# Kernel optimization log

Measured on AMD Instinct MI355X. Metric: run time of the kernel, lower is better.

Reference implementation:

```python
import jax, jax.numpy as jnp
import numpy as np

B, SIZE, TRACK = 4096, 1024, 1024  # batch, input size, tracker_size


def setup_inputs() -> dict:
    key = jax.random.key(0)
    ks = jax.random.split(key, 9)
    s = 0.02  # small init scale to keep gates in a sane range
    return {
        "top_buf_h": jax.random.normal(ks[0], (B, SIZE), jnp.float32),
        "top_stack1_h": jax.random.normal(ks[1], (B, SIZE), jnp.float32),
        "top_stack2_h": jax.random.normal(ks[2], (B, SIZE), jnp.float32),
        "h_prev": jax.random.normal(ks[3], (B, TRACK), jnp.float32),
        "c_prev": jax.random.normal(ks[4], (B, TRACK), jnp.float32),
        "W_buf": jax.random.normal(ks[5], (SIZE, 4 * TRACK), jnp.float32) * s,
        "W_stack1": jax.random.normal(ks[6], (SIZE, 4 * TRACK), jnp.float32) * s,
        "W_stack2": jax.random.normal(ks[7], (SIZE, 4 * TRACK), jnp.float32) * s,
        "W_lateral": jax.random.normal(ks[8], (TRACK, 4 * TRACK), jnp.float32) * s,
        "b_lateral": jnp.zeros((4 * TRACK,), jnp.float32),
    }


def reference(top_buf_h, top_stack1_h, top_stack2_h, h_prev, c_prev,
              W_buf, W_stack1, W_stack2, W_lateral, b_lateral):
    # Fused tracker step: 3 bias-free projections + lateral projection (with bias)
    gates = (top_buf_h @ W_buf
             + top_stack1_h @ W_stack1
             + top_stack2_h @ W_stack2
             + h_prev @ W_lateral
             + b_lateral)                      # [B, 4*TRACK]
    # SPINN lstm(c_prev, gates): chunk order (a, i, f, o)
    a, i, f, o = jnp.split(gates, 4, axis=1)
    c = jnp.tanh(a) * jax.nn.sigmoid(i) + jax.nn.sigmoid(f) * c_prev
    h = jax.nn.sigmoid(o) * jnp.tanh(c)
    return (h, c)
```

## Files before the change

kernel.cpp:

```cpp
#include <hip/hip_runtime.h>


typedef __bf16 bf16x8 __attribute__((ext_vector_type(8)));
typedef float  f32x4  __attribute__((ext_vector_type(4)));

__device__ __forceinline__ unsigned short f2bf(float x) {
    unsigned int u = __builtin_bit_cast(unsigned int, x);
    u = (u + 0x7fffu + ((u >> 16) & 1u)) >> 16;
    return (unsigned short)u;
}

__device__ __forceinline__ void gl2lds16(const unsigned short* g, unsigned short* l) {
    __builtin_amdgcn_global_load_lds(
        (const __attribute__((address_space(1))) unsigned int*)g,
        (__attribute__((address_space(3))) unsigned int*)l,
        16, 0, 0);
}

__device__ __forceinline__ float sigf(float x) {
    return __builtin_amdgcn_rcpf(1.f + __expf(-x));
}
__device__ __forceinline__ float tanh_fast(float x) {
    return 2.f * __builtin_amdgcn_rcpf(1.f + __expf(-2.f * x)) - 1.f;
}


__global__ void convert_AB(const float* __restrict__ A0, const float* __restrict__ A1,
                           const float* __restrict__ A2, const float* __restrict__ A3,
                           const float* __restrict__ Wb, const float* __restrict__ W1,
                           const float* __restrict__ W2, const float* __restrict__ Wl,
                           unsigned short* __restrict__ Abf,
                           unsigned short* __restrict__ Bt) {
    __shared__ float t[32][33];
    if (blockIdx.x < 16384) {
        int idx = blockIdx.x * 256 + threadIdx.x;
        int e0  = idx * 4;
        int b   = e0 >> 12;
        int k   = e0 & 4095;
        const float* S = (k < 1024) ? A0 : (k < 2048) ? A1 : (k < 3072) ? A2 : A3;
        int col = k & 1023;
        const float4 v = *reinterpret_cast<const float4*>(S + (size_t)b * 1024 + col);
        ushort4 o;
        o.x = f2bf(v.x); o.y = f2bf(v.y); o.z = f2bf(v.z); o.w = f2bf(v.w);
        *reinterpret_cast<ushort4*>(Abf + (size_t)b * 4096 + k) = o;
    } else {
        int tile = blockIdx.x - 16384;
        int jt = tile & 127, kt = tile >> 7;
        int j0 = jt * 32, k0 = kt * 32;
        int ksel = k0 >> 10;
        const float* S = (ksel == 0) ? Wb : (ksel == 1) ? W1 : (ksel == 2) ? W2 : Wl;
        int kloc = k0 & 1023;
        int tx = threadIdx.x & 31, ty = threadIdx.x >> 5;
#pragma unroll
        for (int i = 0; i < 4; ++i) {
            int r = ty + i * 8;
            t[r][tx] = S[(size_t)(kloc + r) * 4096 + j0 + tx];
        }
        __syncthreads();
        int g = j0 >> 10;
        int nbase = j0 & 1023;
#pragma unroll
        for (int i = 0; i < 4; ++i) {
            int jj = ty + i * 8;
            int u  = nbase + jj;
            int p  = (u >> 6) * 256 + ((u >> 4) & 3) * 64 + g * 16 + (u & 15);
            Bt[(size_t)p * 4096 + k0 + tx] = f2bf(t[tx][jj]);
        }
    }
}


__global__ __launch_bounds__(512, 2) void gemm_lstm(
        const unsigned short* __restrict__ A,
        const unsigned short* __restrict__ Bt,
        const float* __restrict__ bias,
        const float* __restrict__ cprev,
        float* __restrict__ out) {
    __shared__ unsigned short lds[65536];
#define ASB(b) (lds + (b) * 16384)
#define BSB(b) (lds + 32768 + (b) * 16384)

    const int tid  = threadIdx.x;
    const int wid  = tid >> 6;
    const int lane = tid & 63;
    const int wm = wid >> 2, wn = wid & 3;
    const int lr = lane & 15, lq = lane >> 4;
    const int bm = blockIdx.y, bc = blockIdx.x;

    const int X0 = wid * 1024 + lane * 16;
    const int rs = X0 >> 7;
    const int cs = ((X0 & 127) ^ ((rs & 7) << 4)) >> 1;
    const unsigned short* Agb = A  + ((size_t)(bm * 256 + rs)) * 4096 + cs;
    const unsigned short* Bgb = Bt + ((size_t)(bc * 256 + rs)) * 4096 + cs;

    const int swz = (lr & 7) << 4;
    const int ca0 = ((lq * 16) ^ swz) >> 1;
    const int ca1 = ((64 + lq * 16) ^ swz) >> 1;

    f32x4 acc[8][4] = {};

#define STAGE_A(b, h, kt) do {                                               \
        unsigned short* _d = ASB(b) + (h) * 8192 + wid * 512;                \
        const unsigned short* _s = Agb + (size_t)((h) * 128) * 4096 + (kt) * 64; \
        gl2lds16(_s, _d);                                                    \
        gl2lds16(_s + 64 * 4096, _d + 4096);                                 \
    } while (0)
#define STAGE_B(b, h, kt) do {                                               \
        unsigned short* _d = BSB(b) + (h) * 8192 + wid * 512;                \
        const unsigned short* _s = Bgb + (size_t)((h) * 128) * 4096 + (kt) * 64; \
        gl2lds16(_s, _d);                                                    \
        gl2lds16(_s + 64 * 4096, _d + 4096);                                 \
    } while (0)
#define LDA(buf, mi, cax) (*reinterpret_cast<const bf16x8*>((buf) + (wm * 128 + (mi) * 16 + lr) * 64 + (cax)))
#define LDB(buf, ni, cax) (*reinterpret_cast<const bf16x8*>((buf) + (wn * 64  + (ni) * 16 + lr) * 64 + (cax)))
#define SBAR() __builtin_amdgcn_s_barrier()
#define LGK0() asm volatile("s_waitcnt lgkmcnt(0)")
#define MFMA16(P)                                                            \
        __builtin_amdgcn_s_setprio(1);                                       \
        _Pragma("unroll")                                                    \
        for (int m = 0; m < 2; ++m)                                          \
        _Pragma("unroll")                                                    \
        for (int ks = 0; ks < 2; ++ks)                                       \
        _Pragma("unroll")                                                    \
        for (int ni = 0; ni < 4; ++ni)                                       \
            acc[(P)*2 + m][ni] = __builtin_amdgcn_mfma_f32_16x16x32_bf16(    \
                af[m][ks], bfr[ni][ks], acc[(P)*2 + m][ni], 0, 0, 0);        \
        __builtin_amdgcn_s_setprio(0)

    STAGE_A(0, 0, 0); STAGE_A(0, 1, 0);
    STAGE_B(0, 0, 0); STAGE_B(0, 1, 0);
    STAGE_B(1, 0, 1); STAGE_B(1, 1, 1);
    asm volatile("s_waitcnt vmcnt(4)" ::: "memory");
    SBAR();

#pragma unroll 2
    for (int t = 0; t < 64; ++t) {
        const unsigned short* Ac = ASB(t & 1);
        const unsigned short* Bc = BSB(t & 1);
        const int bn  = (t & 1) ^ 1;
        const int bb  = t & 1;
        const int ktA = (t < 63) ? t + 1 : 63;
        const int ktB = (t < 62) ? t + 2 : 63;

        bf16x8 bfr[4][2];
        {
            bf16x8 af[2][2];
#pragma unroll
            for (int ni = 0; ni < 4; ++ni) { bfr[ni][0] = LDB(Bc, ni, ca0); bfr[ni][1] = LDB(Bc, ni, ca1); }
#pragma unroll
            for (int m = 0; m < 2; ++m) { af[m][0] = LDA(Ac, 0 + m, ca0); af[m][1] = LDA(Ac, 0 + m, ca1); }
            STAGE_A(bn, 0, ktA);
            SBAR();
            LGK0();
            MFMA16(0);
            SBAR();
        }
        {
            bf16x8 af[2][2];
#pragma unroll
            for (int m = 0; m < 2; ++m) { af[m][0] = LDA(Ac, 2 + m, ca0); af[m][1] = LDA(Ac, 2 + m, ca1); }
            STAGE_A(bn, 1, ktA);
            SBAR();
            LGK0();
            MFMA16(1);
            SBAR();
        }
        {
            bf16x8 af[2][2];
#pragma unroll
            for (int m = 0; m < 2; ++m) { af[m][0] = LDA(Ac, 4 + m, ca0); af[m][1] = LDA(Ac, 4 + m, ca1); }
            STAGE_B(bb, 0, ktB);
            SBAR();
            LGK0();
            MFMA16(2);
            SBAR();
        }
        {
            bf16x8 af[2][2];
#pragma unroll
            for (int m = 0; m < 2; ++m) { af[m][0] = LDA(Ac, 6 + m, ca0); af[m][1] = LDA(Ac, 6 + m, ca1); }
            STAGE_B(bb, 1, ktB);
            SBAR();
            LGK0();
            MFMA16(3);
            asm volatile("s_waitcnt vmcnt(4)" ::: "memory");
            SBAR();
        }
    }

    const int u = bc * 64 + wn * 16 + lr;
    const float ba  = bias[u];
    const float bi  = bias[1024 + u];
    const float bfv = bias[2048 + u];
    const float bo  = bias[3072 + u];
    float* outh = out;
    float* outc = out + (size_t)4096 * 1024;

#pragma unroll
    for (int mi = 0; mi < 8; ++mi) {
        const int r0 = bm * 256 + wm * 128 + mi * 16 + lq * 4;
#pragma unroll
        for (int r = 0; r < 4; ++r) {
            const size_t off = (size_t)(r0 + r) * 1024 + u;
            const float a  = acc[mi][0][r] + ba;
            const float ii = acc[mi][1][r] + bi;
            const float ff = acc[mi][2][r] + bfv;
            const float oo = acc[mi][3][r] + bo;
            const float c  = tanh_fast(a) * sigf(ii) + sigf(ff) * cprev[off];
            outh[off] = sigf(oo) * tanh_fast(c);
            outc[off] = c;
        }
    }
#undef STAGE_A
#undef STAGE_B
#undef LDA
#undef LDB
#undef SBAR
#undef LGK0
#undef MFMA16
#undef ASB
#undef BSB
}


extern "C" void kernel_launch(void* const* d_in, const int* in_sizes, int n_in,
                              void* d_out, int out_size, void* d_ws, size_t ws_size,
                              hipStream_t stream) {
    const float* top_buf = (const float*)d_in[0];
    const float* s1      = (const float*)d_in[1];
    const float* s2      = (const float*)d_in[2];
    const float* hprev   = (const float*)d_in[3];
    const float* cprev   = (const float*)d_in[4];
    const float* Wb      = (const float*)d_in[5];
    const float* W1      = (const float*)d_in[6];
    const float* W2      = (const float*)d_in[7];
    const float* Wl      = (const float*)d_in[8];
    const float* bl      = (const float*)d_in[9];

    unsigned short* Abf = (unsigned short*)d_ws;
    unsigned short* Bt  = Abf + (size_t)4096 * 4096;

    convert_AB<<<32768, 256, 0, stream>>>(top_buf, s1, s2, hprev,
                                          Wb, W1, W2, Wl, Abf, Bt);

    dim3 grid(16, 16);
    gemm_lstm<<<grid, 512, 0, stream>>>(Abf, Bt, bl, cprev, (float*)d_out);
}
```

Baseline: 147.1 us.

## Software-pipeline LDS fragment reads ahead of MFMA phases with register double-buffering

Restructures the K loop so that LDS fragment reads for each phase are issued one phase ahead, overlapping with the previous phase's MFMAs. The next iteration's B fragments and first A fragments are read during the last MFMA phase, and the B fragments ping-pong between two register sets. The explicit lgkmcnt(0) waits are removed, which hides LDS latency at the cost of extra VGPRs for the double-buffered fragments and a risk of reduced occupancy or spills.

```diff
diff --git a/kernel.cpp b/kernel.cpp
--- a/kernel.cpp
+++ b/kernel.cpp
@@ -98,6 +98,8 @@
     const int ca1 = ((64 + lq * 16) ^ swz) >> 1;
 
     f32x4 acc[8][4] = {};
+    bf16x8 afA[2][2], afB[2][2], afC[2][2], afD[2][2];
+    bf16x8 bfr0[4][2], bfr1[4][2];
 
 #define STAGE_A(b, h, kt) do {                                               \
         unsigned short* _d = ASB(b) + (h) * 8192 + wid * 512;                \
@@ -113,9 +115,21 @@
     } while (0)
 #define LDA(buf, mi, cax) (*reinterpret_cast<const bf16x8*>((buf) + (wm * 128 + (mi) * 16 + lr) * 64 + (cax)))
 #define LDB(buf, ni, cax) (*reinterpret_cast<const bf16x8*>((buf) + (wn * 64  + (ni) * 16 + lr) * 64 + (cax)))
+#define RD_A(DST, BUF, MI0) do {                                             \
+        _Pragma("unroll")                                                    \
+        for (int m = 0; m < 2; ++m) {                                        \
+            DST[m][0] = LDA(BUF, (MI0) + m, ca0);                            \
+            DST[m][1] = LDA(BUF, (MI0) + m, ca1);                            \
+        } } while (0)
+#define RD_B(DST, BUF) do {                                                  \
+        _Pragma("unroll")                                                    \
+        for (int n = 0; n < 4; ++n) {                                        \
+            DST[n][0] = LDB(BUF, n, ca0);                                    \
+            DST[n][1] = LDB(BUF, n, ca1);                                    \
+        } } while (0)
 #define SBAR() __builtin_amdgcn_s_barrier()
-#define LGK0() asm volatile("s_waitcnt lgkmcnt(0)")
-#define MFMA16(P)                                                            \
+#define VMFENCE() asm volatile("s_waitcnt vmcnt(4)" ::: "memory")
+#define MFMA16(P, AF, BF)                                                    \
         __builtin_amdgcn_s_setprio(1);                                       \
         _Pragma("unroll")                                                    \
         for (int m = 0; m < 2; ++m)                                          \
@@ -124,75 +138,67 @@
         _Pragma("unroll")                                                    \
         for (int ni = 0; ni < 4; ++ni)                                       \
             acc[(P)*2 + m][ni] = __builtin_amdgcn_mfma_f32_16x16x32_bf16(    \
-                af[m][ks], bfr[ni][ks], acc[(P)*2 + m][ni], 0, 0, 0);        \
+                AF[m][ks], BF[ni][ks], acc[(P)*2 + m][ni], 0, 0, 0);         \
         __builtin_amdgcn_s_setprio(0)
+
+#define KITER(T, PAR, BFC, BFN) do {                                         \
+        const unsigned short* Ac = ASB(PAR);                                 \
+        const int ktA = ((T) < 63) ? (T) + 1 : 63;                           \
+        const int ktB = ((T) < 62) ? (T) + 2 : 63;                           \
+             \
+        RD_A(afC, Ac, 4);                                                    \
+        STAGE_A(PAR ^ 1, 0, ktA);                                            \
+        SBAR();                                                              \
+        MFMA16(0, afA, BFC);                                                 \
+        SBAR();                                                              \
+                                \
+        RD_A(afD, Ac, 6);                                                    \
+        STAGE_A(PAR ^ 1, 1, ktA);                                            \
+        SBAR();                                                              \
+        MFMA16(1, afB, BFC);                                                 \
+        SBAR();                                                              \
+                                                \
+        STAGE_B(PAR, 0, ktB);                                                \
+        SBAR();                                                              \
+        MFMA16(2, afC, BFC);                                                 \
+        SBAR();                                                              \
+         \
+        STAGE_B(PAR, 1, ktB);                                                \
+        VMFENCE();                                                           \
+        SBAR();                                                              \
+        __builtin_amdgcn_sched_barrier(0);                                   \
+        {                                                                    \
+            const unsigned short* An = ASB(PAR ^ 1);                         \
+            const unsigned short* Bn = BSB(PAR ^ 1);                         \
+            RD_B(BFN, Bn);                                                   \
+            RD_A(afA, An, 0);                                                \
+            RD_A(afB, An, 2);                                                \
+        }                                                                    \
+        MFMA16(3, afD, BFC);                                                 \
+        SBAR();                                                              \
+    } while (0)
 
     STAGE_A(0, 0, 0); STAGE_A(0, 1, 0);
     STAGE_B(0, 0, 0); STAGE_B(0, 1, 0);
     STAGE_B(1, 0, 1); STAGE_B(1, 1, 1);
-    asm volatile("s_waitcnt vmcnt(4)" ::: "memory");
+    VMFENCE();
     SBAR();
-
-#pragma unroll 2
-    for (int t = 0; t < 64; ++t) {
-        const unsigned short* Ac = ASB(t & 1);
-        const unsigned short* Bc = BSB(t & 1);
-        const int bn  = (t & 1) ^ 1;
-        const int bb  = t & 1;
-        const int ktA = (t < 63) ? t + 1 : 63;
-        const int ktB = (t < 62) ? t + 2 : 63;
-
-        bf16x8 bfr[4][2];
-        {
-            bf16x8 af[2][2];
-#pragma unroll
-            for (int ni = 0; ni < 4; ++ni) { bfr[ni][0] = LDB(Bc, ni, ca0); bfr[ni][1] = LDB(Bc, ni, ca1); }
-#pragma unroll
-            for (int m = 0; m < 2; ++m) { af[m][0] = LDA(Ac, 0 + m, ca0); af[m][1] = LDA(Ac, 0 + m, ca1); }
-            STAGE_A(bn, 0, ktA);
-            SBAR();
-            LGK0();
-            MFMA16(0);
-            SBAR();
-        }
-        {
-            bf16x8 af[2][2];
-#pragma unroll
-            for (int m = 0; m < 2; ++m) { af[m][0] = LDA(Ac, 2 + m, ca0); af[m][1] = LDA(Ac, 2 + m, ca1); }
-            STAGE_A(bn, 1, ktA);
-            SBAR();
-            LGK0();
-            MFMA16(1);
-            SBAR();
-        }
-        {
-            bf16x8 af[2][2];
-#pragma unroll
-            for (int m = 0; m < 2; ++m) { af[m][0] = LDA(Ac, 4 + m, ca0); af[m][1] = LDA(Ac, 4 + m, ca1); }
-            STAGE_B(bb, 0, ktB);
-            SBAR();
-            LGK0();
-            MFMA16(2);
-            SBAR();
-        }
-        {
-            bf16x8 af[2][2];
-#pragma unroll
-            for (int m = 0; m < 2; ++m) { af[m][0] = LDA(Ac, 6 + m, ca0); af[m][1] = LDA(Ac, 6 + m, ca1); }
-            STAGE_B(bb, 1, ktB);
-            SBAR();
-            LGK0();
-            MFMA16(3);
-            asm volatile("s_waitcnt vmcnt(4)" ::: "memory");
-            SBAR();
-        }
+    __builtin_amdgcn_sched_barrier(0);
+    RD_B(bfr0, BSB(0));
+    RD_A(afA, ASB(0), 0);
+    RD_A(afB, ASB(0), 2);
+
+    for (int u = 0; u < 32; ++u) {
+        const int t0 = 2 * u, t1 = 2 * u + 1;
+        KITER(t0, 0, bfr0, bfr1);
+        KITER(t1, 1, bfr1, bfr0);
     }
 
-    const int u = bc * 64 + wn * 16 + lr;
-    const float ba  = bias[u];
-    const float bi  = bias[1024 + u];
-    const float bfv = bias[2048 + u];
-    const float bo  = bias[3072 + u];
+    const int un = bc * 64 + wn * 16 + lr;
+    const float ba  = bias[un];
+    const float bi  = bias[1024 + un];
+    const float bfv = bias[2048 + un];
+    const float bo  = bias[3072 + un];
     float* outh = out;
     float* outc = out + (size_t)4096 * 1024;
 
@@ -201,7 +207,7 @@
         const int r0 = bm * 256 + wm * 128 + mi * 16 + lq * 4;
 #pragma unroll
         for (int r = 0; r < 4; ++r) {
-            const size_t off = (size_t)(r0 + r) * 1024 + u;
+            const size_t off = (size_t)(r0 + r) * 1024 + un;
             const float a  = acc[mi][0][r] + ba;
             const float ii = acc[mi][1][r] + bi;
             const float ff = acc[mi][2][r] + bfv;
@@ -215,9 +221,12 @@
 #undef STAGE_B
 #undef LDA
 #undef LDB
+#undef RD_A
+#undef RD_B
 #undef SBAR
-#undef LGK0
+#undef VMFENCE
 #undef MFMA16
+#undef KITER
 #undef ASB
 #undef BSB
 }
```

New measurement: 259.8 us. +76.6%, slower.
